# Performance work log

Measured on AMD Instinct MI355X. Metric: run time of the kernel, lower is better.

Reference implementation:

```python
import jax, jax.numpy as jnp
import numpy as np


def setup_inputs() -> dict:
    key = jax.random.key(0)
    k1, k2 = jax.random.split(key)
    d, T, n = 256, 8192, 64
    # scale down so exp(ht^T D^T D hj) stays in range, as typical trained D would
    H = jax.random.normal(k1, (d, T), dtype=jnp.float32) * 0.1
    D = jax.random.normal(k2, (n, d), dtype=jnp.float32) * 0.1
    l2 = jnp.ones((), dtype=jnp.float32)
    return {"H": H, "D": D, "l2": l2}


def reference(H, D, l2):
    # H: [d, T], D: [n, d]
    DH = D @ H                                   # [n, T] = D @ H_T.T
    # S[t, j] = h_t^T (D^T D) h_j  == (DH)^T (DH)
    S = jnp.einsum('nt,nj->tj', DH, DH)          # [T, T]
    # beta_j = exp(-0.5 * ||D h_j||^2); row t: attn[t,:] = beta * exp(S[t,:]) / sum
    log_beta = -0.5 * jnp.sum(DH * DH, axis=0)   # [T]
    attn_map = jax.nn.softmax(S + log_beta[None, :], axis=1)  # [T, T]
    Z = l2 * (H @ attn_map)                      # [d, T]
    return Z
```

## Files before the change

kernel.cpp:

```cpp
#include <hip/hip_runtime.h>

#define T_DIM 8192
#define D_DIM 256
#define N_DIM 64
#define LOG2E 1.44269504f

typedef __bf16 bf16x8 __attribute__((ext_vector_type(8)));
typedef __bf16 bf16x4 __attribute__((ext_vector_type(4)));
typedef float f32x16 __attribute__((ext_vector_type(16)));

__device__ __forceinline__ f32x16 zero16() {
  f32x16 v;
#pragma unroll
  for (int i = 0; i < 16; ++i) v[i] = 0.f;
  return v;
}


__global__ __launch_bounds__(256) void k_dh(const float* __restrict__ H,
                                            const float* __restrict__ Dm,
                                            __bf16* __restrict__ DHf,
                                            float* __restrict__ lbe,
                                            float* __restrict__ rowsum) {
  __shared__ __bf16 HlThi[64 * 264];
  __shared__ __bf16 HlTlo[64 * 264];
  __shared__ __bf16 DHs[64 * 72];
  const int tid = threadIdx.x;
  const int t0 = blockIdx.x * 64;
  const int lane = tid & 63;
  const int wave = tid >> 6;
  const int h = lane >> 5;
  const int l31 = lane & 31;
  const float4* H4 = (const float4*)H;
#pragma unroll
  for (int r = 0; r < 16; ++r) {
    int idx = r * 256 + tid;
    int d = idx >> 4, tc = idx & 15;
    float4 v = H4[(size_t)d * (T_DIM / 4) + (t0 >> 2) + tc];
    float vv[4] = {v.x, v.y, v.z, v.w};
#pragma unroll
    for (int i = 0; i < 4; ++i) {
      __bf16 hi = (__bf16)vv[i];
      float lo = vv[i] - (float)hi;
      HlThi[(tc * 4 + i) * 264 + d] = hi;
      HlTlo[(tc * 4 + i) * 264 + d] = (__bf16)lo;
    }
  }
  __syncthreads();
  const int tt = wave & 1, nh = wave >> 1;
  const int m = tt * 32 + l31;
  const int n = nh * 32 + l31;
  f32x16 c = zero16();
  for (int kk = 0; kk < 16; ++kk) {
    bf16x8 ahi = *(const bf16x8*)&HlThi[m * 264 + kk * 16 + h * 8];
    bf16x8 alo = *(const bf16x8*)&HlTlo[m * 264 + kk * 16 + h * 8];
    const float4* dp = (const float4*)(Dm + (size_t)n * 256 + kk * 16 + h * 8);
    float4 b0 = dp[0], b1 = dp[1];
    float bv[8] = {b0.x, b0.y, b0.z, b0.w, b1.x, b1.y, b1.z, b1.w};
    bf16x8 bhi, blo;
#pragma unroll
    for (int i = 0; i < 8; ++i) {
      __bf16 hi = (__bf16)bv[i];
      bhi[i] = hi;
      blo[i] = (__bf16)(bv[i] - (float)hi);
    }
    c = __builtin_amdgcn_mfma_f32_32x32x16_bf16(ahi, bhi, c, 0, 0, 0);
    c = __builtin_amdgcn_mfma_f32_32x32x16_bf16(ahi, blo, c, 0, 0, 0);
    c = __builtin_amdgcn_mfma_f32_32x32x16_bf16(alo, bhi, c, 0, 0, 0);
  }
#pragma unroll
  for (int r = 0; r < 16; ++r) {
    int row = tt * 32 + (r & 3) + 8 * (r >> 2) + 4 * h;
    DHs[row * 72 + n] = (__bf16)c[r];
  }
  __syncthreads();
#pragma unroll
  for (int r = 0; r < 2; ++r) {
    int idx = r * 256 + tid;
    int g = idx >> 8, cc = (idx >> 5) & 7, l = idx & 31;
    bf16x8 w = *(const bf16x8*)&DHs[(g * 32 + l) * 72 + cc * 8];
    *(bf16x8*)(DHf + (size_t)(blockIdx.x * 2 + g) * 2048 + cc * 256 + l * 8) = w;
  }
  if (tid < 64) {
    float s = 0.f;
#pragma unroll
    for (int q = 0; q < 8; ++q) {
      bf16x8 w = *(const bf16x8*)&DHs[tid * 72 + q * 8];
#pragma unroll
      for (int i = 0; i < 8; ++i) { float f = (float)w[i]; s += f * f; }
    }
    lbe[t0 + tid] = -0.5f * s * LOG2E;
    rowsum[t0 + tid] = 0.f;
  }
}

__global__ __launch_bounds__(256, 2) void k_rowsum(const __bf16* __restrict__ DHf,
                                                   const float* __restrict__ lbe,
                                                   float* __restrict__ rowsum) {
  __shared__ float red2[64 * 65];
  const int tid = threadIdx.x;
  const int lane = tid & 63;
  const int wave = tid >> 6;
  const int h = lane >> 5;
  const int tt = wave & 1, jt = wave >> 1;
  const int t0 = (int)(blockIdx.x >> 4) * 64;
  const int jbase = (int)(blockIdx.x & 15) * 512;
  const int Gt = (t0 >> 5) + tt;
  bf16x8 aR[4];
#pragma unroll
  for (int kk = 0; kk < 4; ++kk)
    aR[kk] = *(const bf16x8*)(DHf + (size_t)Gt * 2048 + kk * 512 + lane * 8);
  float racc[16];
#pragma unroll
  for (int r = 0; r < 16; ++r) racc[r] = 0.f;
  for (int jit = 0; jit < 8; ++jit) {
    const size_t Gj = (jbase >> 5) + jit * 2 + jt;
    bf16x8 b[4];
#pragma unroll
    for (int kk = 0; kk < 4; ++kk)
      b[kk] = *(const bf16x8*)(DHf + Gj * 2048 + kk * 512 + lane * 8);
    const float lbv = lbe[jbase + jit * 64 + jt * 32 + (lane & 31)];
    f32x16 s = zero16();
#pragma unroll
    for (int kk = 0; kk < 4; ++kk)
      s = __builtin_amdgcn_mfma_f32_32x32x16_bf16(aR[kk], b[kk], s, 0, 0, 0);
#pragma unroll
    for (int r = 0; r < 16; ++r)
      racc[r] += __builtin_amdgcn_exp2f(__builtin_fmaf(s[r], LOG2E, lbv));
  }
#pragma unroll
  for (int r = 0; r < 16; ++r) {
    int tl = tt * 32 + (r & 3) + 8 * (r >> 2) + 4 * h;
    red2[tl * 65 + jt * 32 + (lane & 31)] = racc[r];
  }
  __syncthreads();
  if (tid < 64) {
    float s = 0.f;
#pragma unroll 8
    for (int c = 0; c < 64; ++c) s += red2[tid * 65 + c];
    atomicAdd(&rowsum[t0 + tid], s);
  }
}

__global__ __launch_bounds__(256) void k_scaleH(const float* __restrict__ H,
                                                const float* __restrict__ rowsum,
                                                __bf16* __restrict__ Hbf_sw,
                                                float* __restrict__ Z) {
  __shared__ float rinvL[64];
  const int tid = threadIdx.x;
  const int bx = blockIdx.x;
  const int tblk = bx >> 1, dh = bx & 1;
  const int t0 = tblk * 64;
  if (tid < 64) rinvL[tid] = 1.0f / rowsum[t0 + tid];
  __syncthreads();
#pragma unroll
  for (int itr = 0; itr < 4; ++itr) {
    int idx = itr * 256 + tid;
    int dl = idx >> 3, tbp = idx & 7;
    int d = dh * 128 + dl;
    int swz = (d ^ (d >> 3)) & 7;
    int tloc = (tbp ^ swz) << 3;
    const float4* hp = (const float4*)(H + (size_t)d * T_DIM + t0 + tloc);
    float4 v0 = hp[0], v1 = hp[1];
    float4 r0 = *(const float4*)&rinvL[tloc];
    float4 r1 = *(const float4*)&rinvL[tloc + 4];
    bf16x8 w;
    w[0] = (__bf16)(v0.x * r0.x); w[1] = (__bf16)(v0.y * r0.y);
    w[2] = (__bf16)(v0.z * r0.z); w[3] = (__bf16)(v0.w * r0.w);
    w[4] = (__bf16)(v1.x * r1.x); w[5] = (__bf16)(v1.y * r1.y);
    w[6] = (__bf16)(v1.z * r1.z); w[7] = (__bf16)(v1.w * r1.w);
    *(bf16x8*)(Hbf_sw + (size_t)tblk * 16384 + (size_t)d * 64 + tbp * 8) = w;
  }
  float4* Z4 = (float4*)Z;
  const int base = bx * 256 + tid;
  const float4 z4 = {0.f, 0.f, 0.f, 0.f};
#pragma unroll
  for (int r = 0; r < 8; ++r) Z4[r * 65536 + base] = z4;
}

__global__ __launch_bounds__(256, 2) void k_z(const __bf16* __restrict__ Hbf_sw,
                                              const __bf16* __restrict__ DHf,
                                              const float* __restrict__ lbe,
                                              const float* __restrict__ l2p,
                                              float* __restrict__ Z) {
  __shared__ __bf16 Hs[2][128 * 64];
  __shared__ __bf16 Pt[2][128 * 64];
  const int tid = threadIdx.x;
  const int lane = tid & 63;
  const int wave = tid >> 6;
  const int h = lane >> 5;
  const int l31 = lane & 31;
  const int bx = blockIdx.x;
  const int ts = bx & 3;
  const int dh = (bx >> 2) & 1;
  const int j0 = (bx >> 3) * 128;
  const float l2v = l2p[0];
  const int s_tt = wave & 1, s_jg = wave >> 1;
  bf16x8 bS[2][4];
  float lbv[2];
#pragma unroll
  for (int q = 0; q < 2; ++q) {
    const size_t Gj = (j0 >> 5) + s_jg * 2 + q;
#pragma unroll
    for (int kk = 0; kk < 4; ++kk)
      bS[q][kk] = *(const bf16x8*)(DHf + Gj * 2048 + kk * 512 + lane * 8);
    lbv[q] = lbe[j0 + (s_jg * 2 + q) * 32 + l31];
  }
  f32x16 acc[2][2];
#pragma unroll
  for (int u = 0; u < 2; ++u)
#pragma unroll
    for (int v = 0; v < 2; ++v) acc[u][v] = zero16();

#define DMA_HS(buf_, it_)                                                       \
  {                                                                             \
    const __bf16* gsrc =                                                        \
        Hbf_sw + (size_t)(ts * 32 + (it_)) * 16384 + (size_t)dh * 8192;         \
    _Pragma("unroll") for (int r = 0; r < 4; ++r) {                             \
      int chunk = wave * 4 + r;                                                 \
      __builtin_amdgcn_global_load_lds(                                         \
          (const __attribute__((address_space(1))) unsigned int*)(gsrc +        \
              chunk * 512 + lane * 8),                                          \
          (__attribute__((address_space(3))) unsigned int*)(&Hs[buf_][0] +      \
              chunk * 512),                                                     \
          16, 0, 0);                                                            \
    }                                                                           \
  }

#define S_PHASE(p_)                                                             \
  {                                                                             \
    _Pragma("unroll") for (int q = 0; q < 2; ++q) {                             \
      f32x16 s = zero16();                                                      \
      _Pragma("unroll") for (int kk = 0; kk < 4; ++kk)                          \
          s = __builtin_amdgcn_mfma_f32_32x32x16_bf16(aR[kk], bS[q][kk], s, 0,  \
                                                      0, 0);                    \
      const int jl = (s_jg * 2 + q) * 32 + l31;                                 \
      const int sj = (jl ^ (jl >> 3)) & 7;                                      \
      _Pragma("unroll") for (int g = 0; g < 4; ++g) {                           \
        const int tl = s_tt * 32 + g * 8 + 4 * h;                               \
        bf16x4 pv;                                                              \
        pv[0] = (__bf16)__builtin_amdgcn_exp2f(                                 \
            __builtin_fmaf(s[g * 4 + 0], LOG2E, lbv[q]));                       \
        pv[1] = (__bf16)__builtin_amdgcn_exp2f(                                 \
            __builtin_fmaf(s[g * 4 + 1], LOG2E, lbv[q]));                       \
        pv[2] = (__bf16)__builtin_amdgcn_exp2f(                                 \
            __builtin_fmaf(s[g * 4 + 2], LOG2E, lbv[q]));                       \
        pv[3] = (__bf16)__builtin_amdgcn_exp2f(                                 \
            __builtin_fmaf(s[g * 4 + 3], LOG2E, lbv[q]));                       \
        const int cchunk = tl >> 3;                                             \
        *(bf16x4*)&Pt[p_][jl * 64 + ((cchunk ^ sj) << 3) + 4 * h] = pv;         \
      }                                                                         \
    }                                                                           \
  }

  bf16x8 aR[4];
#pragma unroll
  for (int kk = 0; kk < 4; ++kk)
    aR[kk] = *(const bf16x8*)(DHf + (size_t)(ts * 64 + s_tt) * 2048 + kk * 512 + lane * 8);
  DMA_HS(0, 0);
  S_PHASE(0);
#pragma unroll
  for (int kk = 0; kk < 4; ++kk)
    aR[kk] = *(const bf16x8*)(DHf + (size_t)(ts * 64 + 2 + s_tt) * 2048 + kk * 512 + lane * 8);
  __syncthreads();

  for (int it = 0; it < 32; ++it) {
    const int p = it & 1;
    if (it < 31) {
      DMA_HS(p ^ 1, it + 1);
      S_PHASE(p ^ 1);
    }
    if (it < 30) {
      const size_t Gt = ts * 64 + (it + 2) * 2 + s_tt;
#pragma unroll
      for (int kk = 0; kk < 4; ++kk)
        aR[kk] = *(const bf16x8*)(DHf + Gt * 2048 + kk * 512 + lane * 8);
    }
#pragma unroll
    for (int kk = 0; kk < 4; ++kk) {
      const int c = kk * 2 + h;
      bf16x8 af[2], bw[2];
#pragma unroll
      for (int u = 0; u < 2; ++u) {
        int dl = (wave & 1) * 64 + u * 32 + l31;
        af[u] = *(const bf16x8*)&Hs[p][dl * 64 + ((c ^ ((dl ^ (dl >> 3)) & 7)) << 3)];
      }
#pragma unroll
      for (int v = 0; v < 2; ++v) {
        int j = (wave >> 1) * 64 + v * 32 + l31;
        bw[v] = *(const bf16x8*)&Pt[p][j * 64 + ((c ^ ((j ^ (j >> 3)) & 7)) << 3)];
      }
#pragma unroll
      for (int u = 0; u < 2; ++u)
#pragma unroll
        for (int v = 0; v < 2; ++v)
          acc[u][v] = __builtin_amdgcn_mfma_f32_32x32x16_bf16(af[u], bw[v], acc[u][v], 0, 0, 0);
    }
    __syncthreads();
  }
#undef S_PHASE
#undef DMA_HS
#pragma unroll
  for (int u = 0; u < 2; ++u)
#pragma unroll
    for (int v = 0; v < 2; ++v)
#pragma unroll
      for (int r = 0; r < 16; ++r) {
        int d = dh * 128 + (wave & 1) * 64 + u * 32 + (r & 3) + 8 * (r >> 2) + 4 * h;
        int j = j0 + (wave >> 1) * 64 + v * 32 + l31;
        atomicAdd(&Z[(size_t)d * T_DIM + j], acc[u][v][r] * l2v);
      }
}

extern "C" void kernel_launch(void* const* d_in, const int* in_sizes, int n_in,
                              void* d_out, int out_size, void* d_ws,
                              size_t ws_size, hipStream_t stream) {
  (void)in_sizes; (void)n_in; (void)out_size; (void)ws_size;
  const float* H = (const float*)d_in[0];
  const float* Dm = (const float*)d_in[1];
  const float* l2 = (const float*)d_in[2];
  float* Z = (float*)d_out;
  char* ws = (char*)d_ws;
  __bf16* DHf = (__bf16*)ws;
  float* lbe = (float*)(ws + 1048576);
  float* rowsum = (float*)(ws + 1048576 + 32768);
  __bf16* Hbf_sw = (__bf16*)(ws + 1048576 + 65536);

  k_dh<<<128, 256, 0, stream>>>(H, Dm, DHf, lbe, rowsum);
  k_rowsum<<<2048, 256, 0, stream>>>(DHf, lbe, rowsum);
  k_scaleH<<<256, 256, 0, stream>>>(H, rowsum, Hbf_sw, Z);
  k_z<<<512, 256, 0, stream>>>(Hbf_sw, DHf, lbe, l2, Z);
}
```

Before: 160.3 us.

## Eliminate k_scaleH by folding row normalization into k_z probabilities

Removes the separate k_scaleH launch. The bf16 swizzled copy of H is now written unscaled in k_dh, and the Z zero-fill moves into k_rowsum. The 1/rowsum factor is applied to each exp probability inside k_z's S phase through a per-iteration reciprocal load. k_rowsum also gains a one-step register prefetch of the next DH tile. This saves a kernel launch and an extra pass over H, at the cost of more multiplies and rowsum loads inside the k_z inner loop.

```diff
diff --git a/kernel.cpp b/kernel.cpp
--- a/kernel.cpp
+++ b/kernel.cpp
@@ -20,6 +20,7 @@
 __global__ __launch_bounds__(256) void k_dh(const float* __restrict__ H,
                                             const float* __restrict__ Dm,
                                             __bf16* __restrict__ DHf,
+                                            __bf16* __restrict__ Hbf_sw,
                                             float* __restrict__ lbe,
                                             float* __restrict__ rowsum) {
   __shared__ __bf16 HlThi[64 * 264];
@@ -38,13 +39,19 @@
     int d = idx >> 4, tc = idx & 15;
     float4 v = H4[(size_t)d * (T_DIM / 4) + (t0 >> 2) + tc];
     float vv[4] = {v.x, v.y, v.z, v.w};
+    bf16x4 whi;
 #pragma unroll
     for (int i = 0; i < 4; ++i) {
       __bf16 hi = (__bf16)vv[i];
       float lo = vv[i] - (float)hi;
+      whi[i] = hi;
       HlThi[(tc * 4 + i) * 264 + d] = hi;
       HlTlo[(tc * 4 + i) * 264 + d] = (__bf16)lo;
     }
+    int tb = tc >> 1, off = (tc & 1) * 4;
+    int swz = (d ^ (d >> 3)) & 7;
+    *(bf16x4*)(Hbf_sw + (size_t)blockIdx.x * 16384 + (size_t)d * 64 +
+               ((tb ^ swz) << 3) + off) = whi;
   }
   __syncthreads();
   const int tt = wave & 1, nh = wave >> 1;
@@ -96,7 +103,8 @@
 
 __global__ __launch_bounds__(256, 2) void k_rowsum(const __bf16* __restrict__ DHf,
                                                    const float* __restrict__ lbe,
-                                                   float* __restrict__ rowsum) {
+                                                   float* __restrict__ rowsum,
+                                                   float* __restrict__ Z) {
   __shared__ float red2[64 * 65];
   const int tid = threadIdx.x;
   const int lane = tid & 63;
@@ -106,6 +114,7 @@
   const int t0 = (int)(blockIdx.x >> 4) * 64;
   const int jbase = (int)(blockIdx.x & 15) * 512;
   const int Gt = (t0 >> 5) + tt;
+  ((float4*)Z)[(size_t)blockIdx.x * 256 + tid] = float4{0.f, 0.f, 0.f, 0.f};
   bf16x8 aR[4];
 #pragma unroll
   for (int kk = 0; kk < 4; ++kk)
@@ -113,17 +122,28 @@
   float racc[16];
 #pragma unroll
   for (int r = 0; r < 16; ++r) racc[r] = 0.f;
+  bf16x8 bN[4];
+  {
+    const size_t Gj0 = (jbase >> 5) + jt;
+#pragma unroll
+    for (int kk = 0; kk < 4; ++kk)
+      bN[kk] = *(const bf16x8*)(DHf + Gj0 * 2048 + kk * 512 + lane * 8);
+  }
   for (int jit = 0; jit < 8; ++jit) {
-    const size_t Gj = (jbase >> 5) + jit * 2 + jt;
-    bf16x8 b[4];
+    bf16x8 bC[4];
+#pragma unroll
+    for (int kk = 0; kk < 4; ++kk) bC[kk] = bN[kk];
+    const float lbv = lbe[jbase + jit * 64 + jt * 32 + (lane & 31)];
+    if (jit < 7) {
+      const size_t Gj = (jbase >> 5) + (jit + 1) * 2 + jt;
+#pragma unroll
+      for (int kk = 0; kk < 4; ++kk)
+        bN[kk] = *(const bf16x8*)(DHf + Gj * 2048 + kk * 512 + lane * 8);
+    }
+    f32x16 s = zero16();
 #pragma unroll
     for (int kk = 0; kk < 4; ++kk)
-      b[kk] = *(const bf16x8*)(DHf + Gj * 2048 + kk * 512 + lane * 8);
-    const float lbv = lbe[jbase + jit * 64 + jt * 32 + (lane & 31)];
-    f32x16 s = zero16();
-#pragma unroll
-    for (int kk = 0; kk < 4; ++kk)
-      s = __builtin_amdgcn_mfma_f32_32x32x16_bf16(aR[kk], b[kk], s, 0, 0, 0);
+      s = __builtin_amdgcn_mfma_f32_32x32x16_bf16(aR[kk], bC[kk], s, 0, 0, 0);
 #pragma unroll
     for (int r = 0; r < 16; ++r)
       racc[r] += __builtin_amdgcn_exp2f(__builtin_fmaf(s[r], LOG2E, lbv));
@@ -142,45 +162,10 @@
   }
 }
 
-__global__ __launch_bounds__(256) void k_scaleH(const float* __restrict__ H,
-                                                const float* __restrict__ rowsum,
-                                                __bf16* __restrict__ Hbf_sw,
-                                                float* __restrict__ Z) {
-  __shared__ float rinvL[64];
-  const int tid = threadIdx.x;
-  const int bx = blockIdx.x;
-  const int tblk = bx >> 1, dh = bx & 1;
-  const int t0 = tblk * 64;
-  if (tid < 64) rinvL[tid] = 1.0f / rowsum[t0 + tid];
-  __syncthreads();
-#pragma unroll
-  for (int itr = 0; itr < 4; ++itr) {
-    int idx = itr * 256 + tid;
-    int dl = idx >> 3, tbp = idx & 7;
-    int d = dh * 128 + dl;
-    int swz = (d ^ (d >> 3)) & 7;
-    int tloc = (tbp ^ swz) << 3;
-    const float4* hp = (const float4*)(H + (size_t)d * T_DIM + t0 + tloc);
-    float4 v0 = hp[0], v1 = hp[1];
-    float4 r0 = *(const float4*)&rinvL[tloc];
-    float4 r1 = *(const float4*)&rinvL[tloc + 4];
-    bf16x8 w;
-    w[0] = (__bf16)(v0.x * r0.x); w[1] = (__bf16)(v0.y * r0.y);
-    w[2] = (__bf16)(v0.z * r0.z); w[3] = (__bf16)(v0.w * r0.w);
-    w[4] = (__bf16)(v1.x * r1.x); w[5] = (__bf16)(v1.y * r1.y);
-    w[6] = (__bf16)(v1.z * r1.z); w[7] = (__bf16)(v1.w * r1.w);
-    *(bf16x8*)(Hbf_sw + (size_t)tblk * 16384 + (size_t)d * 64 + tbp * 8) = w;
-  }
-  float4* Z4 = (float4*)Z;
-  const int base = bx * 256 + tid;
-  const float4 z4 = {0.f, 0.f, 0.f, 0.f};
-#pragma unroll
-  for (int r = 0; r < 8; ++r) Z4[r * 65536 + base] = z4;
-}
-
 __global__ __launch_bounds__(256, 2) void k_z(const __bf16* __restrict__ Hbf_sw,
                                               const __bf16* __restrict__ DHf,
                                               const float* __restrict__ lbe,
+                                              const float* __restrict__ rowsum,
                                               const float* __restrict__ l2p,
                                               float* __restrict__ Z) {
   __shared__ __bf16 Hs[2][128 * 64];
@@ -194,6 +179,7 @@
   const int ts = bx & 3;
   const int dh = (bx >> 2) & 1;
   const int j0 = (bx >> 3) * 128;
+  const int tbase = ts * 2048;
   const float l2v = l2p[0];
   const int s_tt = wave & 1, s_jg = wave >> 1;
   bf16x8 bS[2][4];
@@ -227,6 +213,19 @@
     }                                                                           \
   }
 
+  float4 rvv[4];
+#define LOAD_RVV(it_)                                                           \
+  {                                                                             \
+    _Pragma("unroll") for (int g = 0; g < 4; ++g) {                             \
+      const float4 rs4 = *(const float4*)(rowsum + tbase + (it_) * 64 +         \
+                                          s_tt * 32 + g * 8 + 4 * h);           \
+      rvv[g].x = __builtin_amdgcn_rcpf(rs4.x);                                  \
+      rvv[g].y = __builtin_amdgcn_rcpf(rs4.y);                                  \
+      rvv[g].z = __builtin_amdgcn_rcpf(rs4.z);                                  \
+      rvv[g].w = __builtin_amdgcn_rcpf(rs4.w);                                  \
+    }                                                                           \
+  }
+
 #define S_PHASE(p_)                                                             \
   {                                                                             \
     _Pragma("unroll") for (int q = 0; q < 2; ++q) {                             \
@@ -239,14 +238,14 @@
       _Pragma("unroll") for (int g = 0; g < 4; ++g) {                           \
         const int tl = s_tt * 32 + g * 8 + 4 * h;                               \
         bf16x4 pv;                                                              \
-        pv[0] = (__bf16)__builtin_amdgcn_exp2f(                                 \
-            __builtin_fmaf(s[g * 4 + 0], LOG2E, lbv[q]));                       \
-        pv[1] = (__bf16)__builtin_amdgcn_exp2f(                                 \
-            __builtin_fmaf(s[g * 4 + 1], LOG2E, lbv[q]));                       \
-        pv[2] = (__bf16)__builtin_amdgcn_exp2f(                                 \
-            __builtin_fmaf(s[g * 4 + 2], LOG2E, lbv[q]));                       \
-        pv[3] = (__bf16)__builtin_amdgcn_exp2f(                                 \
-            __builtin_fmaf(s[g * 4 + 3], LOG2E, lbv[q]));                       \
+        pv[0] = (__bf16)(__builtin_amdgcn_exp2f(                                \
+                    __builtin_fmaf(s[g * 4 + 0], LOG2E, lbv[q])) * rvv[g].x);   \
+        pv[1] = (__bf16)(__builtin_amdgcn_exp2f(                                \
+                    __builtin_fmaf(s[g * 4 + 1], LOG2E, lbv[q])) * rvv[g].y);   \
+        pv[2] = (__bf16)(__builtin_amdgcn_exp2f(                                \
+                    __builtin_fmaf(s[g * 4 + 2], LOG2E, lbv[q])) * rvv[g].z);   \
+        pv[3] = (__bf16)(__builtin_amdgcn_exp2f(                                \
+                    __builtin_fmaf(s[g * 4 + 3], LOG2E, lbv[q])) * rvv[g].w);   \
         const int cchunk = tl >> 3;                                             \
         *(bf16x4*)&Pt[p_][jl * 64 + ((cchunk ^ sj) << 3) + 4 * h] = pv;         \
       }                                                                         \
@@ -257,11 +256,13 @@
 #pragma unroll
   for (int kk = 0; kk < 4; ++kk)
     aR[kk] = *(const bf16x8*)(DHf + (size_t)(ts * 64 + s_tt) * 2048 + kk * 512 + lane * 8);
+  LOAD_RVV(0);
   DMA_HS(0, 0);
   S_PHASE(0);
 #pragma unroll
   for (int kk = 0; kk < 4; ++kk)
     aR[kk] = *(const bf16x8*)(DHf + (size_t)(ts * 64 + 2 + s_tt) * 2048 + kk * 512 + lane * 8);
+  LOAD_RVV(1);
   __syncthreads();
 
   for (int it = 0; it < 32; ++it) {
@@ -275,6 +276,7 @@
 #pragma unroll
       for (int kk = 0; kk < 4; ++kk)
         aR[kk] = *(const bf16x8*)(DHf + Gt * 2048 + kk * 512 + lane * 8);
+      LOAD_RVV(it + 2);
     }
 #pragma unroll
     for (int kk = 0; kk < 4; ++kk) {
@@ -299,6 +301,7 @@
     __syncthreads();
   }
 #undef S_PHASE
+#undef LOAD_RVV
 #undef DMA_HS
 #pragma unroll
   for (int u = 0; u < 2; ++u)
@@ -326,8 +329,7 @@
   float* rowsum = (float*)(ws + 1048576 + 32768);
   __bf16* Hbf_sw = (__bf16*)(ws + 1048576 + 65536);
 
-  k_dh<<<128, 256, 0, stream>>>(H, Dm, DHf, lbe, rowsum);
-  k_rowsum<<<2048, 256, 0, stream>>>(DHf, lbe, rowsum);
-  k_scaleH<<<256, 256, 0, stream>>>(H, rowsum, Hbf_sw, Z);
-  k_z<<<512, 256, 0, stream>>>(Hbf_sw, DHf, lbe, l2, Z);
-}
+  k_dh<<<128, 256, 0, stream>>>(H, Dm, DHf, Hbf_sw, lbe, rowsum);
+  k_rowsum<<<2048, 256, 0, stream>>>(DHf, lbe, rowsum, Z);
+  k_z<<<512, 256, 0, stream>>>(Hbf_sw, DHf, lbe, rowsum, l2, Z);
+}
```

After: 164.1 us. 2.4% more time.
